# Kernel tuning notes

Measured on AMD Instinct MI355X. Metric: run time of the kernel, lower is better.

Reference implementation:

```python
import jax, jax.numpy as jnp
import numpy as np

# Mamba hyperparams (standard defaults: expand=2, d_conv=4, dt_rank=ceil(d_model/16))
D_MODEL = 256
D_STATE = 16
D_CONV = 4
D_INNER = 2 * D_MODEL  # 512
DT_RANK = (D_MODEL + 15) // 16  # 16
B, H, W = 2, 64, 64


def setup_inputs() -> dict:
    key = jax.random.key(0)
    ks = jax.random.split(key, 8)
    def rnd(k, shape, scale):
        return jax.random.normal(k, shape, jnp.float32) * scale
    A_log = jnp.log(jnp.tile(jnp.arange(1, D_STATE + 1, dtype=jnp.float32), (D_INNER, 1)))
    return {
        "x": jax.random.normal(ks[0], (B, D_MODEL, H, W), jnp.float32),
        "W_in": rnd(ks[1], (D_MODEL, 2 * D_INNER), 0.02),
        "conv_w": rnd(ks[2], (D_INNER, 1, D_CONV), 0.1),
        "conv_b": jnp.zeros((D_INNER,), jnp.float32),
        "W_x": rnd(ks[3], (D_INNER, DT_RANK + 2 * D_STATE), 0.02),
        "W_dt": rnd(ks[4], (DT_RANK, D_INNER), 0.02),
        "b_dt": rnd(ks[5], (D_INNER,), 0.1),
        "A_log": A_log,
        "D": jnp.ones((D_INNER,), jnp.float32),
        "W_out": rnd(ks[6], (D_INNER, D_MODEL), 0.02),
    }


def _mamba(z, W_in, conv_w, conv_b, W_x, W_dt, b_dt, A_log, Dp, W_out):
    # z: (Bt, L, d_model)
    Bt = z.shape[0]
    xz = z @ W_in                              # (Bt, L, 2*d_inner)
    xm, gate = jnp.split(xz, 2, axis=-1)
    # causal depthwise conv1d (kernel D_CONV, left-padded)
    xc = jnp.transpose(xm, (0, 2, 1))          # (Bt, d_inner, L)
    xc = jnp.pad(xc, ((0, 0), (0, 0), (D_CONV - 1, 0)))
    xc = jax.lax.conv_general_dilated(
        xc, conv_w, (1,), 'VALID',
        dimension_numbers=('NCH', 'OIH', 'NCH'),
        feature_group_count=D_INNER)
    xc = xc + conv_b[None, :, None]
    xs = jax.nn.silu(jnp.transpose(xc, (0, 2, 1)))   # (Bt, L, d_inner)
    dbl = xs @ W_x                                     # (Bt, L, dt_rank + 2*d_state)
    dt = jax.nn.softplus(dbl[..., :DT_RANK] @ W_dt + b_dt)  # (Bt, L, d_inner)
    Bm = dbl[..., DT_RANK:DT_RANK + D_STATE]           # (Bt, L, d_state)
    Cm = dbl[..., DT_RANK + D_STATE:]                  # (Bt, L, d_state)
    A = -jnp.exp(A_log)                                # (d_inner, d_state)

    def step(state, ins):
        dt_t, B_t, C_t, x_t = ins                      # (Bt,d_inner),(Bt,d_state),(Bt,d_state),(Bt,d_inner)
        dA = jnp.exp(dt_t[..., None] * A)              # (Bt, d_inner, d_state)
        state = dA * state + (dt_t * x_t)[..., None] * B_t[:, None, :]
        y_t = jnp.einsum('bds,bs->bd', state, C_t)
        return state, y_t

    tm = lambda a: jnp.moveaxis(a, 1, 0)               # time-major
    init = jnp.zeros((Bt, D_INNER, D_STATE), z.dtype)
    _, ys = jax.lax.scan(step, init, (tm(dt), tm(Bm), tm(Cm), tm(xs)))
    y = jnp.moveaxis(ys, 0, 1) + xs * Dp               # skip via D
    y = y * jax.nn.silu(gate)
    return y @ W_out                                   # (Bt, L, d_model)


def reference(x, W_in, conv_w, conv_b, W_x, W_dt, b_dt, A_log, D, W_out):
    b, c, h, w = x.shape
    l = h * w
    # four scan directions: identity, flip w, flip h, flip both
    zs = jnp.stack([x,
                    jnp.flip(x, 3),
                    jnp.flip(x, 2),
                    jnp.flip(x, (2, 3))], axis=0)       # (4, b, c, h, w)
    zs = zs.reshape(4 * b, c, l).transpose(0, 2, 1)     # (4b, l, c)
    y = _mamba(zs, W_in, conv_w, conv_b, W_x, W_dt, b_dt, A_log, D, W_out)
    y = y.transpose(0, 2, 1).reshape(4, b, c, h, w)
    y0 = y[0]
    y1 = jnp.flip(y[1], 3)
    y2 = jnp.flip(y[2], 2)
    y3 = jnp.flip(y[3], (2, 3))
    return (y0 + y1 + y2 + y3) / 4.0
```

## Files before the change

kernel.cpp:

```cpp
#include <hip/hip_runtime.h>
#include <cstdint>
#include <cstddef>

#define LSEQ 4096
#define DI   512
#define NSTATE 16
#define TC 64
#define NCH 64

#define XZ_OFF  0
#define XS_OFF  33554432
#define DBL_OFF 50331648
#define AP_OFF  51904512
#define PS_OFF  56098816

typedef unsigned short u16;
typedef __attribute__((ext_vector_type(8))) short s8v;
typedef __attribute__((ext_vector_type(4))) float f4v;
typedef __attribute__((ext_vector_type(4))) unsigned int u32x4;

#ifndef __has_builtin
#define __has_builtin(x) 0
#endif
#if __has_builtin(__builtin_amdgcn_global_load_lds)
#define USE_GLL 1
#else
#define USE_GLL 0
#endif

__device__ __forceinline__ float silu_f(float v) { return v / (1.f + __expf(-v)); }
__device__ __forceinline__ float softplus_f(float v) {
  return fmaxf(v, 0.f) + log1pf(__expf(-fabsf(v)));
}
__device__ __forceinline__ u16 bf16_hi(float v) {
  unsigned u = __float_as_uint(v);
  return (u16)((u + 0x7fffu + ((u >> 16) & 1u)) >> 16);
}
__device__ __forceinline__ float bf16_f(u16 h) { return __uint_as_float(((unsigned)h) << 16); }

__device__ __forceinline__ void gld16(const u16* g, u16* l, int lane) {
#if USE_GLL
  __builtin_amdgcn_global_load_lds((const __attribute__((address_space(1))) void*)g,
                                   (__attribute__((address_space(3))) void*)l, 16, 0, 0);
#else
  *(u32x4*)(l + lane * 8) = *(const u32x4*)g;
#endif
}

__device__ __forceinline__ void pow_ladder(float r, float* a) {
  const float r2 = r * r, r4 = r2 * r2, r8 = r4 * r4;
  a[0] = r;        a[1] = r2;       a[2] = r2 * r;   a[3] = r4;
  a[4] = r4 * r;   a[5] = r4 * r2;  a[6] = r4 * a[2]; a[7] = r8;
  a[8] = r8 * r;   a[9] = r8 * r2;  a[10] = r8 * a[2]; a[11] = r8 * r4;
  a[12] = r8 * a[4]; a[13] = r8 * a[5]; a[14] = r8 * a[6]; a[15] = r8 * r8;
}

__global__ __launch_bounds__(256) void k_split(const float* __restrict__ in,
                                               u16* __restrict__ oh,
                                               u16* __restrict__ ol,
                                               int R, int C) {
  __shared__ float tile[64][65];
  const size_t zoff = (size_t)blockIdx.z * R * C;
  in += zoff; oh += zoff; ol += zoff;
  const int c0 = blockIdx.x << 6, r0 = blockIdx.y << 6;
  const int tid = threadIdx.x;
  const int tx = tid & 63, ty = tid >> 6;
#pragma unroll
  for (int i = 0; i < 16; ++i) {
    const int r = ty + (i << 2);
    tile[r][tx] = in[(size_t)(r0 + r) * C + c0 + tx];
  }
  __syncthreads();
#pragma unroll
  for (int i = 0; i < 16; ++i) {
    const int cc = ty + (i << 2);
    const float v = tile[tx][cc];
    const u16 h = bf16_hi(v);
    const size_t o = (size_t)(c0 + cc) * R + r0 + tx;
    oh[o] = h;
    ol[o] = bf16_hi(v - bf16_f(h));
  }
}

__global__ __launch_bounds__(256) void k_gemm_in_mfma(const u16* __restrict__ xTh,
                                                      const u16* __restrict__ xTl,
                                                      const u16* __restrict__ Wh,
                                                      const u16* __restrict__ Wl,
                                                      float* __restrict__ xz) {
  __shared__ __attribute__((aligned(16))) u16 lds[4 * 128 * 32];
  u16* Ah = lds;
  u16* Al = lds + 4096;
  u16* Bh = lds + 8192;
  u16* Bl = lds + 12288;
  const int rt = blockIdx.x;
  const int nt = blockIdx.y;
  const int seq = rt >> 5, hl2 = rt & 31;
  const int b = seq & 1, dir = seq >> 1;
  const int tid = threadIdx.x;
  const int lane = tid & 63, wid = tid >> 6;
  const int wr = wid >> 1, wc = wid & 1;

  const u16* gsrc = (wid == 0) ? xTh : (wid == 1) ? xTl : (wid == 2) ? Wh : Wl;
  u16* ldst = lds + (wid << 12);
  size_t roff[8];
#pragma unroll
  for (int i = 0; i < 8; ++i) {
    const int r = (i << 4) + (lane >> 2);
    size_t off;
    if (wid < 2) {
      const int hl = (hl2 << 1) + (r >> 6), w = r & 63;
      const int hp = (dir & 2) ? 63 - hl : hl;
      const int wp = (dir & 1) ? 63 - w : w;
      off = ((size_t)((b << 12) + (hp << 6) + wp)) << 8;
    } else {
      off = ((size_t)((nt << 7) + r)) << 8;
    }
    roff[i] = off + ((lane & 3) << 3);
  }

  f4v acc[4][4];
  const f4v z4 = {0.f, 0.f, 0.f, 0.f};
#pragma unroll
  for (int m = 0; m < 4; ++m)
#pragma unroll
    for (int n = 0; n < 4; ++n) acc[m][n] = z4;

  const int fr = lane & 15;
  const int kg = (lane >> 4) << 3;

  for (int kc = 0; kc < 256; kc += 32) {
    __syncthreads();
#pragma unroll
    for (int i = 0; i < 8; ++i) gld16(gsrc + roff[i] + kc, ldst + (i << 9), lane);
    __syncthreads();
    s8v Afh[4], Afl[4], Bfh[4], Bfl[4];
#pragma unroll
    for (int m = 0; m < 4; ++m) {
      const int row = (wr << 6) + (m << 4) + fr;
      Afh[m] = *(const s8v*)&Ah[row * 32 + kg];
      Afl[m] = *(const s8v*)&Al[row * 32 + kg];
    }
#pragma unroll
    for (int n = 0; n < 4; ++n) {
      const int row = (wc << 6) + (n << 4) + fr;
      Bfh[n] = *(const s8v*)&Bh[row * 32 + kg];
      Bfl[n] = *(const s8v*)&Bl[row * 32 + kg];
    }
#pragma unroll
    for (int m = 0; m < 4; ++m)
#pragma unroll
      for (int n = 0; n < 4; ++n) {
        acc[m][n] = __builtin_amdgcn_mfma_f32_16x16x32_bf16(Afh[m], Bfh[n], acc[m][n], 0, 0, 0);
        acc[m][n] = __builtin_amdgcn_mfma_f32_16x16x32_bf16(Afh[m], Bfl[n], acc[m][n], 0, 0, 0);
        acc[m][n] = __builtin_amdgcn_mfma_f32_16x16x32_bf16(Afl[m], Bfh[n], acc[m][n], 0, 0, 0);
      }
  }
  const int rg = (lane >> 4) << 2;
  float* obase = xz + ((size_t)((rt << 7) + (wr << 6) + rg)) * 1024 + (nt << 7) + (wc << 6) + fr;
#pragma unroll
  for (int m = 0; m < 4; ++m)
#pragma unroll
    for (int n = 0; n < 4; ++n)
#pragma unroll
      for (int j = 0; j < 4; ++j)
        obase[(size_t)((m << 4) + j) * 1024 + (n << 4)] = acc[m][n][j];
}

__global__ __launch_bounds__(256) void k_conv(const float* __restrict__ xz,
                                              const float* __restrict__ cw,
                                              const float* __restrict__ cb,
                                              float* __restrict__ xs) {
  const int t0  = blockIdx.x << 4;
  const int seq = blockIdx.y;
  const int d   = (blockIdx.z << 8) + threadIdx.x;
  const float* xm = xz + (size_t)seq * LSEQ * 1024 + d;
  const float w0 = cw[d * 4], w1 = cw[d * 4 + 1], w2 = cw[d * 4 + 2], w3 = cw[d * 4 + 3];
  const float bias = cb[d];
  float r0 = (t0 >= 3) ? xm[(size_t)(t0 - 3) * 1024] : 0.f;
  float r1 = (t0 >= 2) ? xm[(size_t)(t0 - 2) * 1024] : 0.f;
  float r2 = (t0 >= 1) ? xm[(size_t)(t0 - 1) * 1024] : 0.f;
  float* orow = xs + ((size_t)seq * LSEQ + t0) * DI + d;
#pragma unroll
  for (int i = 0; i < 16; ++i) {
    const float r3 = xm[(size_t)(t0 + i) * 1024];
    const float v = fmaf(w0, r0, fmaf(w1, r1, fmaf(w2, r2, fmaf(w3, r3, bias))));
    orow[(size_t)i * DI] = silu_f(v);
    r0 = r1; r1 = r2; r2 = r3;
  }
}

__global__ __launch_bounds__(256) void k_gemm_x(const float* __restrict__ xs,
                                                const float* __restrict__ Wx,
                                                float* __restrict__ dbl) {
  __shared__ float xsh[16][512];
  const int rb  = blockIdx.x;
  const int tid = threadIdx.x;
  const int r = tid >> 4, k4 = tid & 15;
  const float* src = xs + (size_t)rb * 16 * DI;
#pragma unroll
  for (int i = 0; i < 8; ++i) {
    const int k = (i << 6) + (k4 << 2);
    *(float4*)&xsh[r][k] = *(const float4*)&src[(size_t)r * DI + k];
  }
  __syncthreads();
  if (tid < 192) {
    const int col = tid % 48;
    const int rg  = tid / 48;
    float a0 = 0.f, a1 = 0.f, a2 = 0.f, a3 = 0.f;
    for (int k = 0; k < 512; k += 4) {
      float wv0 = Wx[(size_t)(k + 0) * 48 + col];
      float wv1 = Wx[(size_t)(k + 1) * 48 + col];
      float wv2 = Wx[(size_t)(k + 2) * 48 + col];
      float wv3 = Wx[(size_t)(k + 3) * 48 + col];
      const float4 x0 = *(const float4*)&xsh[rg * 4 + 0][k];
      const float4 x1 = *(const float4*)&xsh[rg * 4 + 1][k];
      const float4 x2 = *(const float4*)&xsh[rg * 4 + 2][k];
      const float4 x3 = *(const float4*)&xsh[rg * 4 + 3][k];
      a0 = fmaf(x0.x, wv0, fmaf(x0.y, wv1, fmaf(x0.z, wv2, fmaf(x0.w, wv3, a0))));
      a1 = fmaf(x1.x, wv0, fmaf(x1.y, wv1, fmaf(x1.z, wv2, fmaf(x1.w, wv3, a1))));
      a2 = fmaf(x2.x, wv0, fmaf(x2.y, wv1, fmaf(x2.z, wv2, fmaf(x2.w, wv3, a2))));
      a3 = fmaf(x3.x, wv0, fmaf(x3.y, wv1, fmaf(x3.z, wv2, fmaf(x3.w, wv3, a3))));
    }
    const size_t base = ((size_t)rb * 16 + rg * 4) * 48 + col;
    dbl[base] = a0; dbl[base + 48] = a1; dbl[base + 96] = a2; dbl[base + 144] = a3;
  }
}

__global__ __launch_bounds__(256) void k_scan1(const float* __restrict__ xs,
                                               const float* __restrict__ dbl,
                                               const float* __restrict__ Wdt,
                                               const float* __restrict__ bdt,
                                               const float* __restrict__ Alog,
                                               float* __restrict__ aprod,
                                               float* __restrict__ pstate) {
  __shared__ float dsh[TC * 48];
  const int ch = blockIdx.x, seq = blockIdx.y;
  const int tid = threadIdx.x;
  const int d = (blockIdx.z << 8) + tid;
  const int t0 = ch << 6;
  const float* dsrc = dbl + ((size_t)seq * LSEQ + t0) * 48;
#pragma unroll
  for (int i = 0; i < 12; ++i) dsh[tid + (i << 8)] = dsrc[tid + (i << 8)];
  float wdt[16], Aa[16], st[16], P[16];
#pragma unroll
  for (int k = 0; k < 16; ++k) wdt[k] = Wdt[(size_t)k * DI + d];
  const float bd = bdt[d];
  bool fast = true;
#pragma unroll
  for (int s = 0; s < NSTATE; ++s) {
    const float Av = __expf(Alog[d * NSTATE + s]);
    Aa[s] = -Av;
    fast = fast && (fabsf(Av - (float)(s + 1)) < 1e-3f);
    st[s] = 0.f; P[s] = 1.f;
  }
  const float* xsrc = xs + ((size_t)seq * LSEQ + t0) * DI + d;
  __syncthreads();
  if (fast) {
    float Rp = 1.f;
    for (int t = 0; t < TC; ++t) {
      const float* dr = &dsh[t * 48];
      float dtp = bd;
#pragma unroll
      for (int k = 0; k < 16; ++k) dtp = fmaf(dr[k], wdt[k], dtp);
      const float dtv = softplus_f(dtp);
      const float u = dtv * xsrc[(size_t)t * DI];
      const float r = __expf(-dtv);
      float a[16];
      pow_ladder(r, a);
      Rp *= r;
#pragma unroll
      for (int s = 0; s < NSTATE; ++s) st[s] = fmaf(a[s], st[s], u * dr[16 + s]);
    }
    pow_ladder(Rp, P);
  } else {
    for (int t = 0; t < TC; ++t) {
      const float* dr = &dsh[t * 48];
      float dtp = bd;
#pragma unroll
      for (int k = 0; k < 16; ++k) dtp = fmaf(dr[k], wdt[k], dtp);
      const float dtv = softplus_f(dtp);
      const float u = dtv * xsrc[(size_t)t * DI];
#pragma unroll
      for (int s = 0; s < NSTATE; ++s) {
        const float a = __expf(dtv * Aa[s]);
        st[s] = fmaf(a, st[s], u * dr[16 + s]);
        P[s] *= a;
      }
    }
  }
  float* ap = aprod  + (((size_t)seq * NCH + ch) * DI + d) * NSTATE;
  float* pp = pstate + (((size_t)seq * NCH + ch) * DI + d) * NSTATE;
#pragma unroll
  for (int s = 0; s < NSTATE; s += 4) {
    *(float4*)&ap[s] = make_float4(P[s], P[s + 1], P[s + 2], P[s + 3]);
    *(float4*)&pp[s] = make_float4(st[s], st[s + 1], st[s + 2], st[s + 3]);
  }
}

__global__ __launch_bounds__(256) void k_scan2(const float* __restrict__ aprod,
                                               float* __restrict__ pstate) {
  const int flat = blockIdx.x * 256 + threadIdx.x;
  const int seq = flat >> 13;
  const int rem = flat & 8191;
  const size_t stride = (size_t)DI * NSTATE;
  const size_t base = (size_t)seq * NCH * stride + rem;
  float h = 0.f;
  for (int ch = 0; ch < NCH; ++ch) {
    const size_t o = base + (size_t)ch * stride;
    const float a = aprod[o];
    const float bsum = pstate[o];
    pstate[o] = h;
    h = fmaf(a, h, bsum);
  }
}

__global__ __launch_bounds__(256) void k_scan3(const float* __restrict__ xz,
                                               float* __restrict__ xs,
                                               const float* __restrict__ dbl,
                                               const float* __restrict__ Wdt,
                                               const float* __restrict__ bdt,
                                               const float* __restrict__ Alog,
                                               const float* __restrict__ Dv,
                                               const float* __restrict__ hinit) {
  __shared__ float dsh[TC * 48];
  const int ch = blockIdx.x, seq = blockIdx.y;
  const int tid = threadIdx.x;
  const int d = (blockIdx.z << 8) + tid;
  const int t0 = ch << 6;
  const float* dsrc = dbl + ((size_t)seq * LSEQ + t0) * 48;
#pragma unroll
  for (int i = 0; i < 12; ++i) dsh[tid + (i << 8)] = dsrc[tid + (i << 8)];
  float wdt[16], Aa[16], st[16];
#pragma unroll
  for (int k = 0; k < 16; ++k) wdt[k] = Wdt[(size_t)k * DI + d];
  const float bd = bdt[d];
  const float Dp = Dv[d];
  const float* hp = hinit + (((size_t)seq * NCH + ch) * DI + d) * NSTATE;
  bool fast = true;
#pragma unroll
  for (int s = 0; s < NSTATE; ++s) {
    const float Av = __expf(Alog[d * NSTATE + s]);
    Aa[s] = -Av;
    fast = fast && (fabsf(Av - (float)(s + 1)) < 1e-3f);
    st[s] = hp[s];
  }
  float* xrow = xs + ((size_t)seq * LSEQ + t0) * DI + d;
  const float* grow = xz + ((size_t)seq * LSEQ + t0) * 1024 + 512 + d;
  __syncthreads();
  if (fast) {
    for (int t = 0; t < TC; ++t) {
      const float* dr = &dsh[t * 48];
      float dtp = bd;
#pragma unroll
      for (int k = 0; k < 16; ++k) dtp = fmaf(dr[k], wdt[k], dtp);
      const float dtv = softplus_f(dtp);
      const float xsv = xrow[(size_t)t * DI];
      const float u = dtv * xsv;
      const float r = __expf(-dtv);
      float a[16];
      pow_ladder(r, a);
      float y = 0.f;
#pragma unroll
      for (int s = 0; s < NSTATE; ++s) {
        st[s] = fmaf(a[s], st[s], u * dr[16 + s]);
        y = fmaf(st[s], dr[32 + s], y);
      }
      y = fmaf(xsv, Dp, y);
      const float g = grow[(size_t)t * 1024];
      y *= silu_f(g);
      xrow[(size_t)t * DI] = y;
    }
  } else {
    for (int t = 0; t < TC; ++t) {
      const float* dr = &dsh[t * 48];
      float dtp = bd;
#pragma unroll
      for (int k = 0; k < 16; ++k) dtp = fmaf(dr[k], wdt[k], dtp);
      const float dtv = softplus_f(dtp);
      const float xsv = xrow[(size_t)t * DI];
      const float u = dtv * xsv;
      float y = 0.f;
#pragma unroll
      for (int s = 0; s < NSTATE; ++s) {
        const float a = __expf(dtv * Aa[s]);
        st[s] = fmaf(a, st[s], u * dr[16 + s]);
        y = fmaf(st[s], dr[32 + s], y);
      }
      y = fmaf(xsv, Dp, y);
      const float g = grow[(size_t)t * 1024];
      y *= silu_f(g);
      xrow[(size_t)t * DI] = y;
    }
  }
}

__global__ __launch_bounds__(256) void k_gemm_out(const float* __restrict__ y,
                                                  const float* __restrict__ Wout,
                                                  float* __restrict__ out) {
  __shared__ float smem[64 * 64 + 64 * 128];
  float* Ash = smem;
  float* Bsh = smem + 64 * 64;
  const int bt = blockIdx.x;
  const int b = bt >> 6, tt = bt & 63;
  const int t0 = tt << 6;
  const int c0 = blockIdx.y << 7;
  const int tid = threadIdx.x;
  const int rq = tid >> 4, k4 = tid & 15;
  const int cq = tid & 31, dr8 = tid >> 5;
  const int tx = tid & 31, ty = tid >> 5;
  const int hf = (63 - tt) << 6;
  float acc[8][4];
#pragma unroll
  for (int i = 0; i < 8; ++i)
#pragma unroll
    for (int j = 0; j < 4; ++j) acc[i][j] = 0.f;

  for (int kc = 0; kc < 512; kc += 64) {
#pragma unroll
    for (int i = 0; i < 4; ++i) {
      const int row = rq + (i << 4);
      const int wf = 63 - row;
      const size_t off = kc + (k4 << 2);
      const float4 v0 = *(const float4*)&y[(((size_t)(0 + b) * LSEQ) + t0 + row) * DI + off];
      const float4 v1 = *(const float4*)&y[(((size_t)(2 + b) * LSEQ) + t0 + wf)  * DI + off];
      const float4 v2 = *(const float4*)&y[(((size_t)(4 + b) * LSEQ) + hf + row) * DI + off];
      const float4 v3 = *(const float4*)&y[(((size_t)(6 + b) * LSEQ) + hf + wf)  * DI + off];
      float4 av;
      av.x = 0.25f * (v0.x + v1.x + v2.x + v3.x);
      av.y = 0.25f * (v0.y + v1.y + v2.y + v3.y);
      av.z = 0.25f * (v0.z + v1.z + v2.z + v3.z);
      av.w = 0.25f * (v0.w + v1.w + v2.w + v3.w);
      *(float4*)&Ash[row * 64 + (k4 << 2)] = av;
    }
#pragma unroll
    for (int i = 0; i < 8; ++i) {
      const int kk = dr8 + (i << 3);
      *(float4*)&Bsh[kk * 128 + cq * 4] =
          *(const float4*)&Wout[(size_t)(kc + kk) * 256 + c0 + cq * 4];
    }
    __syncthreads();
#pragma unroll
    for (int kk = 0; kk < 64; ++kk) {
      const float4 bv = *(const float4*)&Bsh[kk * 128 + tx * 4];
      const float br[4] = {bv.x, bv.y, bv.z, bv.w};
#pragma unroll
      for (int i = 0; i < 8; ++i) {
        const float av = Ash[(ty * 8 + i) * 64 + kk];
#pragma unroll
        for (int j = 0; j < 4; ++j) acc[i][j] = fmaf(av, br[j], acc[i][j]);
      }
    }
    __syncthreads();
  }
  float* Clds = smem;
  __syncthreads();
#pragma unroll
  for (int i = 0; i < 8; ++i)
#pragma unroll
    for (int j = 0; j < 4; ++j) Clds[(tx * 4 + j) * 65 + ty * 8 + i] = acc[i][j];
  __syncthreads();
#pragma unroll
  for (int rr = 0; rr < 32; ++rr) {
    const int idx = rr * 256 + tid;
    const int cl = idx >> 6, tl = idx & 63;
    out[((size_t)b * 256 + c0 + cl) * LSEQ + t0 + tl] = Clds[cl * 65 + tl];
  }
}

extern "C" void kernel_launch(void* const* d_in, const int* in_sizes, int n_in,
                              void* d_out, int out_size, void* d_ws, size_t ws_size,
                              hipStream_t stream) {
  const float* x     = (const float*)d_in[0];
  const float* W_in  = (const float*)d_in[1];
  const float* convw = (const float*)d_in[2];
  const float* convb = (const float*)d_in[3];
  const float* W_x   = (const float*)d_in[4];
  const float* W_dt  = (const float*)d_in[5];
  const float* b_dt  = (const float*)d_in[6];
  const float* A_log = (const float*)d_in[7];
  const float* Dvec  = (const float*)d_in[8];
  const float* W_out = (const float*)d_in[9];
  float* out = (float*)d_out;

  float* ws  = (float*)d_ws;
  float* xz  = ws + XZ_OFF;
  float* xs  = ws + XS_OFF;
  float* dbl = ws + DBL_OFF;
  float* ap  = ws + AP_OFF;
  float* ps  = ws + PS_OFF;

  u16* xTh   = (u16*)ap;
  u16* xTl   = xTh + 2097152;
  u16* WinTh = xTl + 2097152;
  u16* WinTl = WinTh + 262144;

  k_split<<<dim3(64, 4, 2), 256, 0, stream>>>(x, xTh, xTl, 256, 4096);
  k_split<<<dim3(16, 4, 1), 256, 0, stream>>>(W_in, WinTh, WinTl, 256, 1024);
  k_gemm_in_mfma<<<dim3(256, 8), 256, 0, stream>>>(xTh, xTl, WinTh, WinTl, xz);
  k_conv<<<dim3(256, 8, 2), 256, 0, stream>>>(xz, convw, convb, xs);
  k_gemm_x<<<dim3(2048), 256, 0, stream>>>(xs, W_x, dbl);
  k_scan1<<<dim3(NCH, 8, 2), 256, 0, stream>>>(xs, dbl, W_dt, b_dt, A_log, ap, ps);
  k_scan2<<<dim3(256), 256, 0, stream>>>(ap, ps);
  k_scan3<<<dim3(NCH, 8, 2), 256, 0, stream>>>(xz, xs, dbl, W_dt, b_dt, A_log, Dvec, ps);
  k_gemm_out<<<dim3(128, 2), 256, 0, stream>>>(xs, W_out, out);
}
```

Measured before the change: 490.2 us.

## Halve scan chunk length, split xz into xm/gate buffers, use fast silu/softplus

The scan chunk length drops from 64 to 32 and the chunk count rises to 128, so the scan1 and scan3 passes launch twice as many blocks. The in-projection GEMM now writes separate contiguous xm and gate buffers with row stride 512 instead of one interleaved 1024-wide buffer, which should improve locality for the conv and scan3 reads. The ap/ps scratch is moved to reuse the xm region, which is no longer needed once conv has run. silu and softplus switch to reciprocal and __logf fast-math forms, trading a little accuracy for fewer instructions, and the longer serial pass over chunks in scan2 adds some overhead.

```diff
diff --git a/kernel.cpp b/kernel.cpp
--- a/kernel.cpp
+++ b/kernel.cpp
@@ -5,14 +5,16 @@
 #define LSEQ 4096
 #define DI   512
 #define NSTATE 16
-#define TC 64
-#define NCH 64
-
-#define XZ_OFF  0
-#define XS_OFF  33554432
-#define DBL_OFF 50331648
-#define AP_OFF  51904512
-#define PS_OFF  56098816
+#define TC 32
+#define NCH 128
+
+#define XM_OFF    0
+#define GATE_OFF  16777216
+#define XS_OFF    33554432
+#define DBL_OFF   50331648
+#define SPLIT_OFF 51904512
+#define AP_OFF    0
+#define PS_OFF    8388608
 
 typedef unsigned short u16;
 typedef __attribute__((ext_vector_type(8))) short s8v;
@@ -28,9 +30,11 @@
 #define USE_GLL 0
 #endif
 
-__device__ __forceinline__ float silu_f(float v) { return v / (1.f + __expf(-v)); }
+__device__ __forceinline__ float silu_f(float v) {
+  return v * __frcp_rn(1.f + __expf(-v));
+}
 __device__ __forceinline__ float softplus_f(float v) {
-  return fmaxf(v, 0.f) + log1pf(__expf(-fabsf(v)));
+  return fmaxf(v, 0.f) + __logf(1.f + __expf(-fabsf(v)));
 }
 __device__ __forceinline__ u16 bf16_hi(float v) {
   unsigned u = __float_as_uint(v);
@@ -86,7 +90,8 @@
                                                       const u16* __restrict__ xTl,
                                                       const u16* __restrict__ Wh,
                                                       const u16* __restrict__ Wl,
-                                                      float* __restrict__ xz) {
+                                                      float* __restrict__ xm,
+                                                      float* __restrict__ gate) {
   __shared__ __attribute__((aligned(16))) u16 lds[4 * 128 * 32];
   u16* Ah = lds;
   u16* Al = lds + 4096;
@@ -156,33 +161,35 @@
       }
   }
   const int rg = (lane >> 4) << 2;
-  float* obase = xz + ((size_t)((rt << 7) + (wr << 6) + rg)) * 1024 + (nt << 7) + (wc << 6) + fr;
+  float* obuf = (nt & 4) ? gate : xm;
+  const int ncol = (nt & 3) << 7;
+  float* obase = obuf + ((size_t)((rt << 7) + (wr << 6) + rg)) * DI + ncol + (wc << 6) + fr;
 #pragma unroll
   for (int m = 0; m < 4; ++m)
 #pragma unroll
     for (int n = 0; n < 4; ++n)
 #pragma unroll
       for (int j = 0; j < 4; ++j)
-        obase[(size_t)((m << 4) + j) * 1024 + (n << 4)] = acc[m][n][j];
-}
-
-__global__ __launch_bounds__(256) void k_conv(const float* __restrict__ xz,
+        obase[(size_t)((m << 4) + j) * DI + (n << 4)] = acc[m][n][j];
+}
+
+__global__ __launch_bounds__(256) void k_conv(const float* __restrict__ xmb,
                                               const float* __restrict__ cw,
                                               const float* __restrict__ cb,
                                               float* __restrict__ xs) {
   const int t0  = blockIdx.x << 4;
   const int seq = blockIdx.y;
   const int d   = (blockIdx.z << 8) + threadIdx.x;
-  const float* xm = xz + (size_t)seq * LSEQ * 1024 + d;
+  const float* xm = xmb + (size_t)seq * LSEQ * DI + d;
   const float w0 = cw[d * 4], w1 = cw[d * 4 + 1], w2 = cw[d * 4 + 2], w3 = cw[d * 4 + 3];
   const float bias = cb[d];
-  float r0 = (t0 >= 3) ? xm[(size_t)(t0 - 3) * 1024] : 0.f;
-  float r1 = (t0 >= 2) ? xm[(size_t)(t0 - 2) * 1024] : 0.f;
-  float r2 = (t0 >= 1) ? xm[(size_t)(t0 - 1) * 1024] : 0.f;
+  float r0 = (t0 >= 3) ? xm[(size_t)(t0 - 3) * DI] : 0.f;
+  float r1 = (t0 >= 2) ? xm[(size_t)(t0 - 2) * DI] : 0.f;
+  float r2 = (t0 >= 1) ? xm[(size_t)(t0 - 1) * DI] : 0.f;
   float* orow = xs + ((size_t)seq * LSEQ + t0) * DI + d;
 #pragma unroll
   for (int i = 0; i < 16; ++i) {
-    const float r3 = xm[(size_t)(t0 + i) * 1024];
+    const float r3 = xm[(size_t)(t0 + i) * DI];
     const float v = fmaf(w0, r0, fmaf(w1, r1, fmaf(w2, r2, fmaf(w3, r3, bias))));
     orow[(size_t)i * DI] = silu_f(v);
     r0 = r1; r1 = r2; r2 = r3;
@@ -237,10 +244,10 @@
   const int ch = blockIdx.x, seq = blockIdx.y;
   const int tid = threadIdx.x;
   const int d = (blockIdx.z << 8) + tid;
-  const int t0 = ch << 6;
+  const int t0 = ch * TC;
   const float* dsrc = dbl + ((size_t)seq * LSEQ + t0) * 48;
 #pragma unroll
-  for (int i = 0; i < 12; ++i) dsh[tid + (i << 8)] = dsrc[tid + (i << 8)];
+  for (int i = 0; i < 6; ++i) dsh[tid + (i << 8)] = dsrc[tid + (i << 8)];
   float wdt[16], Aa[16], st[16], P[16];
 #pragma unroll
   for (int k = 0; k < 16; ++k) wdt[k] = Wdt[(size_t)k * DI + d];
@@ -314,7 +321,7 @@
   }
 }
 
-__global__ __launch_bounds__(256) void k_scan3(const float* __restrict__ xz,
+__global__ __launch_bounds__(256) void k_scan3(const float* __restrict__ gate,
                                                float* __restrict__ xs,
                                                const float* __restrict__ dbl,
                                                const float* __restrict__ Wdt,
@@ -326,10 +333,10 @@
   const int ch = blockIdx.x, seq = blockIdx.y;
   const int tid = threadIdx.x;
   const int d = (blockIdx.z << 8) + tid;
-  const int t0 = ch << 6;
+  const int t0 = ch * TC;
   const float* dsrc = dbl + ((size_t)seq * LSEQ + t0) * 48;
 #pragma unroll
-  for (int i = 0; i < 12; ++i) dsh[tid + (i << 8)] = dsrc[tid + (i << 8)];
+  for (int i = 0; i < 6; ++i) dsh[tid + (i << 8)] = dsrc[tid + (i << 8)];
   float wdt[16], Aa[16], st[16];
 #pragma unroll
   for (int k = 0; k < 16; ++k) wdt[k] = Wdt[(size_t)k * DI + d];
@@ -345,7 +352,7 @@
     st[s] = hp[s];
   }
   float* xrow = xs + ((size_t)seq * LSEQ + t0) * DI + d;
-  const float* grow = xz + ((size_t)seq * LSEQ + t0) * 1024 + 512 + d;
+  const float* grow = gate + ((size_t)seq * LSEQ + t0) * DI + d;
   __syncthreads();
   if (fast) {
     for (int t = 0; t < TC; ++t) {
@@ -366,8 +373,7 @@
         y = fmaf(st[s], dr[32 + s], y);
       }
       y = fmaf(xsv, Dp, y);
-      const float g = grow[(size_t)t * 1024];
-      y *= silu_f(g);
+      y *= silu_f(grow[(size_t)t * DI]);
       xrow[(size_t)t * DI] = y;
     }
   } else {
@@ -387,8 +393,7 @@
         y = fmaf(st[s], dr[32 + s], y);
       }
       y = fmaf(xsv, Dp, y);
-      const float g = grow[(size_t)t * 1024];
-      y *= silu_f(g);
+      y *= silu_f(grow[(size_t)t * DI]);
       xrow[(size_t)t * DI] = y;
     }
   }
@@ -482,25 +487,26 @@
   const float* W_out = (const float*)d_in[9];
   float* out = (float*)d_out;
 
-  float* ws  = (float*)d_ws;
-  float* xz  = ws + XZ_OFF;
-  float* xs  = ws + XS_OFF;
-  float* dbl = ws + DBL_OFF;
-  float* ap  = ws + AP_OFF;
-  float* ps  = ws + PS_OFF;
-
-  u16* xTh   = (u16*)ap;
+  float* ws   = (float*)d_ws;
+  float* xm   = ws + XM_OFF;
+  float* gate = ws + GATE_OFF;
+  float* xs   = ws + XS_OFF;
+  float* dbl  = ws + DBL_OFF;
+  float* ap   = ws + AP_OFF;
+  float* ps   = ws + PS_OFF;
+
+  u16* xTh   = (u16*)(ws + SPLIT_OFF);
   u16* xTl   = xTh + 2097152;
   u16* WinTh = xTl + 2097152;
   u16* WinTl = WinTh + 262144;
 
   k_split<<<dim3(64, 4, 2), 256, 0, stream>>>(x, xTh, xTl, 256, 4096);
   k_split<<<dim3(16, 4, 1), 256, 0, stream>>>(W_in, WinTh, WinTl, 256, 1024);
-  k_gemm_in_mfma<<<dim3(256, 8), 256, 0, stream>>>(xTh, xTl, WinTh, WinTl, xz);
-  k_conv<<<dim3(256, 8, 2), 256, 0, stream>>>(xz, convw, convb, xs);
+  k_gemm_in_mfma<<<dim3(256, 8), 256, 0, stream>>>(xTh, xTl, WinTh, WinTl, xm, gate);
+  k_conv<<<dim3(256, 8, 2), 256, 0, stream>>>(xm, convw, convb, xs);
   k_gemm_x<<<dim3(2048), 256, 0, stream>>>(xs, W_x, dbl);
   k_scan1<<<dim3(NCH, 8, 2), 256, 0, stream>>>(xs, dbl, W_dt, b_dt, A_log, ap, ps);
   k_scan2<<<dim3(256), 256, 0, stream>>>(ap, ps);
-  k_scan3<<<dim3(NCH, 8, 2), 256, 0, stream>>>(xz, xs, dbl, W_dt, b_dt, A_log, Dvec, ps);
+  k_scan3<<<dim3(NCH, 8, 2), 256, 0, stream>>>(gate, xs, dbl, W_dt, b_dt, A_log, Dvec, ps);
   k_gemm_out<<<dim3(128, 2), 256, 0, stream>>>(xs, W_out, out);
 }
```

Result: faster. 438.1 us (-10.6%).
